# Kernel optimization log

Hardware: AMD Instinct MI355X
Metric: run time of the kernel (lower is better)

The kernel has to match this reference:

```python
import math
import jax, jax.numpy as jnp
import numpy as np

B, S, H, NH = 4, 2048, 1024, 16
HD = H // NH  # 64


def _rope_cos_sin(seq_len, dim, base=10000.0):
    # freqs[j] = base^(-2j/dim), angles = outer(t, freqs)
    inv = 1.0 / (base ** (jnp.arange(0, dim, 2, dtype=jnp.float32) / dim))
    t = jnp.arange(seq_len, dtype=jnp.float32)
    ang = jnp.outer(t, inv)  # (S, dim//2)
    return jnp.cos(ang), jnp.sin(ang)


def _apply_rope(x, cos, sin):
    # x: (B, S, NH, HD); pairs are (x[2i], x[2i+1]) per torch view_as_complex on reshape(..., -1, 2)
    xr = x.reshape(*x.shape[:-1], HD // 2, 2)
    x0, x1 = xr[..., 0], xr[..., 1]
    c = cos[None, :, None, :]  # (1, S, 1, HD//2)
    s = sin[None, :, None, :]
    o0 = x0 * c - x1 * s
    o1 = x0 * s + x1 * c
    return jnp.stack([o0, o1], axis=-1).reshape(x.shape)


def setup_inputs() -> dict:
    key = jax.random.key(0)
    ks = jax.random.split(key, 5)
    scale = 1.0 / math.sqrt(H)
    return {
        "x": jax.random.normal(ks[0], (B, S, H), dtype=jnp.float32),
        "wq": jax.random.normal(ks[1], (H, H), dtype=jnp.float32) * scale,
        "wk": jax.random.normal(ks[2], (H, H), dtype=jnp.float32) * scale,
        "wv": jax.random.normal(ks[3], (H, H), dtype=jnp.float32) * scale,
        "wo": jax.random.normal(ks[4], (H, H), dtype=jnp.float32) * scale,
        "attention_mask": jnp.ones((B, S), dtype=jnp.int32),
    }


def reference(x, wq, wk, wv, wo, attention_mask):
    # Linear(bias=False): y = x @ W.T with W shape (out, in)
    q = jnp.einsum('bsh,oh->bso', x, wq).reshape(B, S, NH, HD)
    k = jnp.einsum('bsh,oh->bso', x, wk).reshape(B, S, NH, HD)
    v = jnp.einsum('bsh,oh->bso', x, wv).reshape(B, S, NH, HD)
    cos, sin = _rope_cos_sin(S, HD)
    q = _apply_rope(q, cos, sin)
    k = _apply_rope(k, cos, sin)
    # scores: (B, NH, S, S)
    scores = jnp.einsum('bqhd,bkhd->bhqk', q, k) / math.sqrt(HD)
    mask = attention_mask[:, None, None, :]  # (B,1,1,S)
    scores = jnp.where(mask == 0, -jnp.inf, scores)
    attn = jax.nn.softmax(scores, axis=-1)
    # attn_dropout: eval mode / p=0 -> identity
    out = jnp.einsum('bhqk,bkhd->bqhd', attn, v).reshape(B, S, H)
    return jnp.einsum('bsh,oh->bso', out, wo)
```

## Files before the change

kernel.cpp:

```cpp
#include <hip/hip_runtime.h>
#include <hip/hip_bf16.h>

#define B_   4
#define S_   2048
#define H_   1024
#define NH_  16
#define HD_  64
#define M_   8192
#define K_   1024

using bf16x8 = __bf16 __attribute__((ext_vector_type(8)));
using f32x4  = float __attribute__((ext_vector_type(4)));
using f32x16 = float __attribute__((ext_vector_type(16)));

__device__ inline f32x4 mfma16(bf16x8 a, bf16x8 b, f32x4 c) {
    return __builtin_amdgcn_mfma_f32_16x16x32_bf16(a, b, c, 0, 0, 0);
}
__device__ inline f32x16 mfma32(bf16x8 a, bf16x8 b, f32x16 c) {
    return __builtin_amdgcn_mfma_f32_32x32x16_bf16(a, b, c, 0, 0, 0);
}

__device__ inline unsigned short f2bf(float f) {
    __hip_bfloat16 h = __float2bfloat16(f);
    return *reinterpret_cast<unsigned short*>(&h);
}

__device__ inline unsigned cvt_pk_bf16(float lo, float hi) {
    unsigned r;
    asm("v_cvt_pk_bf16_f32 %0, %1, %2" : "=v"(r) : "v"(lo), "v"(hi));
    return r;
}

__device__ inline void perm32swap(unsigned &a, unsigned &b) {
    asm("v_permlane32_swap_b32 %0, %1" : "+v"(a), "+v"(b));
}

__device__ inline void gload_lds16(const unsigned short* g, unsigned short* l) {
    __builtin_amdgcn_global_load_lds(
        (const __attribute__((address_space(1))) void*)g,
        (__attribute__((address_space(3))) void*)l, 16, 0, 0);
}

#define EXP2F(x) __builtin_amdgcn_exp2f(x)


__global__ __launch_bounds__(256) void prep_convert(
    const float* __restrict__ x,  const float* __restrict__ wq,
    const float* __restrict__ wk, const float* __restrict__ wv,
    const float* __restrict__ wo, unsigned short* __restrict__ ws,
    const int* __restrict__ mask, float2* __restrict__ ropeb,
    float* __restrict__ biasb, int* __restrict__ kflagb)
{
    size_t u = (size_t)blockIdx.x * 256 + threadIdx.x;
    if (u < 3145728) {
        const float* src; unsigned short* dst; size_t off;
        if (u < 2097152)      { src = x;  dst = ws;            off = u * 4; }
        else if (u < 2359296) { src = wq; dst = ws + 8388608;  off = (u - 2097152) * 4; }
        else if (u < 2621440) { src = wk; dst = ws + 9437184;  off = (u - 2359296) * 4; }
        else if (u < 2883584) { src = wv; dst = ws + 10485760; off = (u - 2621440) * 4; }
        else                  { src = wo; dst = ws + 11534336; off = (u - 2883584) * 4; }
        float4 v = *reinterpret_cast<const float4*>(src + off);
        ushort4 o;
        o.x = f2bf(v.x); o.y = f2bf(v.y); o.z = f2bf(v.z); o.w = f2bf(v.w);
        *reinterpret_cast<ushort4*>(dst + off) = o;
    } else {
        int idx = (int)(u - 3145728);
        int pos = idx >> 5, i = idx & 31;
        float inv = expf(-(float)(2 * i) * (9.210340371976184f / 64.0f));
        float ang = (float)pos * inv;
        float2 cs; cs.x = cosf(ang); cs.y = sinf(ang);
        ropeb[idx] = cs;
        if (idx < B_ * S_)
            biasb[idx] = mask[idx] ? 0.0f : -__builtin_inff();
        if (idx < B_ * 32) {
            int b = idx >> 5, kt = idx & 31;
            int all = 1;
            for (int j = 0; j < 64; j++)
                all &= (mask[b * S_ + kt * 64 + j] != 0) ? 1 : 0;
            kflagb[idx] = all;
        }
    }
}

template<int MODE>
__global__ __launch_bounds__(256, 2) void gemm_main(
    const unsigned short* __restrict__ A,
    const unsigned short* __restrict__ W,
    unsigned short* __restrict__ qbuf, unsigned short* __restrict__ kbuf,
    unsigned short* __restrict__ vtb, float* __restrict__ fout,
    const float* __restrict__ ropeb)
{
    __shared__ alignas(16) unsigned short Al[2][128 * 64];
    __shared__ alignas(16) unsigned short Bl[2][128 * 64];

    const int t = threadIdx.x;
    const int l = t & 63;
    const int w = t >> 6;
    const int lane_r = l & 15, lane_g = l >> 4;
    const int bn = blockIdx.x, bm = blockIdx.y;
    const size_t rowbase = (size_t)bm * 128;
    const int colbase = bn * 128;
    const int wm = (w >> 1) * 64, wn = (w & 1) * 64;
    const int which = (MODE == 0) ? (colbase >> 10) : 3;
    const float scale = (which == 0) ? 0.18033688089184827f : 1.0f;

    const int glrow  = l >> 3;
    const int glslot = (l & 7) ^ glrow;
    const unsigned short* ga = A + (rowbase + w * 8 + glrow) * K_ + glslot * 8;
    const unsigned short* gb = W + (size_t)(colbase + w * 8 + glrow) * K_ + glslot * 8;

#define GLA(bi, kt, i) gload_lds16(ga + (size_t)(i) * 32 * K_ + (kt) * 64, \
                                   &Al[bi][((i) * 32 + w * 8) * 64]);
#define GLB(bi, kt, i) gload_lds16(gb + (size_t)(i) * 32 * K_ + (kt) * 64, \
                                   &Bl[bi][((i) * 32 + w * 8) * 64]);
#define RDA(mt, kk) { int rowa = wm + (mt) * 16 + lane_r;                      \
    af[mt][kk] = *reinterpret_cast<const bf16x8*>((const char*)Al[cur] +       \
        ((rowa * 128 + (kk) * 64 + lane_g * 16) ^ ((rowa & 7) << 4))); }
#define RDB(nt, kk) { int rowb = wn + (nt) * 16 + lane_r;                      \
    bfr[nt][kk] = *reinterpret_cast<const bf16x8*>((const char*)Bl[cur] +      \
        ((rowb * 128 + (kk) * 64 + lane_g * 16) ^ ((rowb & 7) << 4))); }
#define MM(mb, nb)                                                             \
    if (MODE == 0 && which <= 1) {                                             \
        _Pragma("unroll")                                                      \
        for (int a = (nb); a < (nb) + 2; a++)                                  \
            _Pragma("unroll")                                                  \
            for (int b2 = (mb); b2 < (mb) + 2; b2++) {                         \
                acc[a][b2] = mfma16(bfr[a][0], af[b2][0], acc[a][b2]);         \
                acc[a][b2] = mfma16(bfr[a][1], af[b2][1], acc[a][b2]);         \
            }                                                                  \
    } else {                                                                   \
        _Pragma("unroll")                                                      \
        for (int mt = (mb); mt < (mb) + 2; mt++)                               \
            _Pragma("unroll")                                                  \
            for (int nt = (nb); nt < (nb) + 2; nt++) {                         \
                acc[mt][nt] = mfma16(af[mt][0], bfr[nt][0], acc[mt][nt]);      \
                acc[mt][nt] = mfma16(af[mt][1], bfr[nt][1], acc[mt][nt]);      \
            }                                                                  \
    }
#define BARS __builtin_amdgcn_s_barrier();                                     \
             asm volatile("s_waitcnt lgkmcnt(0)" ::: "memory");                \
             __builtin_amdgcn_s_setprio(1);
#define BARE __builtin_amdgcn_s_setprio(0); __builtin_amdgcn_s_barrier();

    f32x4 zero4 = {0.f, 0.f, 0.f, 0.f};
    f32x4 acc[4][4];
#pragma unroll
    for (int a = 0; a < 4; a++)
#pragma unroll
        for (int b2 = 0; b2 < 4; b2++) acc[a][b2] = zero4;

    GLA(0, 0, 0) GLA(0, 0, 1) GLA(0, 0, 2) GLA(0, 0, 3)
    GLB(0, 0, 0) GLB(0, 0, 1) GLB(0, 0, 2) GLB(0, 0, 3)
    __syncthreads();

    for (int kt = 0; kt < 16; kt++) {
        const int cur = kt & 1, nxt = cur ^ 1;
        const bool pf = (kt < 15);
        bf16x8 af[4][2], bfr[4][2];
        RDA(0, 0) RDA(0, 1) RDA(1, 0) RDA(1, 1)
        RDB(0, 0) RDB(0, 1) RDB(1, 0) RDB(1, 1)
        if (pf) { GLA(nxt, kt + 1, 0) GLA(nxt, kt + 1, 1) GLA(nxt, kt + 1, 2) }
        BARS MM(0, 0) BARE
        RDB(2, 0) RDB(2, 1) RDB(3, 0) RDB(3, 1)
        if (pf) { GLA(nxt, kt + 1, 3) GLB(nxt, kt + 1, 0) GLB(nxt, kt + 1, 1) }
        BARS MM(0, 2) BARE
        RDA(2, 0) RDA(2, 1) RDA(3, 0) RDA(3, 1)
        if (pf) { GLB(nxt, kt + 1, 2) GLB(nxt, kt + 1, 3) }
        BARS MM(2, 2) BARE
        __builtin_amdgcn_s_setprio(1);
        MM(2, 0)
        __builtin_amdgcn_s_setprio(0);
        asm volatile("s_waitcnt vmcnt(0)" ::: "memory");
        __builtin_amdgcn_s_barrier();
    }
#undef GLA
#undef GLB
#undef RDA
#undef RDB
#undef MM
#undef BARS
#undef BARE

    if (MODE == 1) {
        float* out = fout;
#pragma unroll
        for (int mt = 0; mt < 4; mt++)
#pragma unroll
            for (int nt = 0; nt < 4; nt++)
#pragma unroll
                for (int i = 0; i < 4; i++) {
                    size_t r = rowbase + wm + mt * 16 + lane_g * 4 + i;
                    int n = colbase + wn + nt * 16 + lane_r;
                    out[r * 1024 + n] = acc[mt][nt][i];
                }
    } else if (which <= 1) {
        unsigned short* out = which ? kbuf : qbuf;
#pragma unroll
        for (int a = 0; a < 4; a++) {
            int nbase = (colbase & 1023) + wn + a * 16 + 4 * lane_g;
            int h = nbase >> 6, d0 = nbase & 63;
#pragma unroll
            for (int b2 = 0; b2 < 4; b2++) {
                size_t r = rowbase + wm + b2 * 16 + lane_r;
                int bb  = (int)(r >> 11);
                int pos = (int)(r & 2047);
                float4 cs = *reinterpret_cast<const float4*>(
                    ropeb + pos * 64 + d0);
                float a0 = acc[a][b2][0], a1 = acc[a][b2][1];
                float a2 = acc[a][b2][2], a3 = acc[a][b2][3];
                float o0 = (a0 * cs.x - a1 * cs.y) * scale;
                float o1 = (a0 * cs.y + a1 * cs.x) * scale;
                float o2 = (a2 * cs.z - a3 * cs.w) * scale;
                float o3 = (a2 * cs.w + a3 * cs.z) * scale;
                uint2 o;
                o.x = cvt_pk_bf16(o0, o1);
                o.y = cvt_pk_bf16(o2, o3);
                *reinterpret_cast<uint2*>(
                    out + (((size_t)(bb * NH_ + h)) * S_ + pos) * 64 + d0) = o;
            }
        }
    } else {
#pragma unroll
        for (int a = 0; a < 4; a++)
#pragma unroll
            for (int b2 = 0; b2 < 4; b2++) {
                size_t rr = rowbase + wm + a * 16 + lane_g * 4;
                int n = (colbase & 1023) + wn + b2 * 16 + lane_r;
                int bb  = (int)(rr >> 11);
                int pos = (int)(rr & 2047);
                int h = n >> 6, d = n & 63;
                ushort4 o;
                o.x = f2bf(acc[a][b2][0]); o.y = f2bf(acc[a][b2][1]);
                o.z = f2bf(acc[a][b2][2]); o.w = f2bf(acc[a][b2][3]);
                *reinterpret_cast<ushort4*>(
                    vtb + (((size_t)(bb * NH_ + h)) * 64 + d) * S_ + pos) = o;
            }
    }
}

__global__ __launch_bounds__(256, 2) void attn_fwd(
    const unsigned short* __restrict__ qb, const unsigned short* __restrict__ kb,
    const unsigned short* __restrict__ vt, const float* __restrict__ biasb,
    const int* __restrict__ kflagb, unsigned short* __restrict__ ao)
{
    __shared__ alignas(16) unsigned short Kl[2][64 * 64];
    __shared__ alignas(16) unsigned short Vl[2][64 * 64];

    const int bid = blockIdx.x;
    const int xcd = bid & 7, idx = bid >> 3;
    const int bh = xcd * 8 + (idx >> 3);
    const int qt = idx & 7;
    const int b = bh >> 4, h = bh & 15;

    const int t = threadIdx.x, l = t & 63, w = t >> 6;
    const int lr = l & 31;
    const int hi = l >> 5;
    const int row8 = lr & 7;

    const unsigned short* qp = qb + (size_t)bh * S_ * 64;
    const unsigned short* kp = kb + (size_t)bh * S_ * 64;
    const unsigned short* vp = vt + (size_t)bh * 64 * S_;
    const float* bp = biasb + (size_t)b * S_;
    const int* kfl = kflagb + b * 32;

    bf16x8 qf[2][4];
#pragma unroll
    for (int qbk = 0; qbk < 2; qbk++) {
        int qrow = qt * 256 + w * 64 + qbk * 32 + lr;
#pragma unroll
        for (int ks = 0; ks < 4; ks++)
            qf[qbk][ks] = *reinterpret_cast<const bf16x8*>(
                qp + (size_t)qrow * 64 + ks * 16 + hi * 8);
    }

    f32x16 zero16;
#pragma unroll
    for (int r = 0; r < 16; r++) zero16[r] = 0.f;

    f32x16 oacc[2][2];
#pragma unroll
    for (int qbk = 0; qbk < 2; qbk++)
#pragma unroll
        for (int r = 0; r < 16; r++) { oacc[qbk][0][r] = 0.f; oacc[qbk][1][r] = 0.f; }
    float lsum[2] = {0.f, 0.f};

    const int grr = l >> 3;
    const int gss = ((l & 7) ^ grr) * 8;

#define STAGE(bi, kt)                                                          \
    {                                                                          \
        _Pragma("unroll")                                                      \
        for (int c = 0; c < 2; c++) {                                          \
            int rbase = w * 16 + c * 8;                                        \
            gload_lds16(kp + (size_t)((kt) * 64 + rbase + grr) * 64 + gss,     \
                        &Kl[bi][rbase * 64]);                                  \
            gload_lds16(vp + (size_t)(rbase + grr) * S_ + (kt) * 64 + gss,     \
                        &Vl[bi][rbase * 64]);                                  \
        }                                                                      \
    }

#define QKBLOCK(C0, C1)                                                        \
    {                                                                          \
        __builtin_amdgcn_s_setprio(1);                                         \
        _Pragma("unroll")                                                      \
        for (int T = 0; T < 2; T++) {                                          \
            int rowb = (32 * T + lr) * 128;                                    \
            bf16x8 kf0 = *reinterpret_cast<const bf16x8*>(                     \
                (const char*)Kl[cur] + rowb + ((hi ^ row8) << 4));             \
            sacc[0][T] = mfma32(kf0, qf[0][0], T ? (C1) : (C0));               \
            sacc[1][T] = mfma32(kf0, qf[1][0], T ? (C1) : (C0));               \
            _Pragma("unroll")                                                  \
            for (int ks = 1; ks < 4; ks++) {                                   \
                bf16x8 kfk = *reinterpret_cast<const bf16x8*>(                 \
                    (const char*)Kl[cur] + rowb + (((2 * ks + hi) ^ row8) << 4)); \
                sacc[0][T] = mfma32(kfk, qf[0][ks], sacc[0][T]);               \
                sacc[1][T] = mfma32(kfk, qf[1][ks], sacc[1][T]);               \
            }                                                                  \
        }                                                                      \
        __builtin_amdgcn_s_setprio(0);                                         \
    }

    STAGE(0, 0)

    for (int kt = 0; kt < 32; kt++) {
        const int cur = kt & 1;
        __syncthreads();
        if (kt < 31) STAGE(cur ^ 1, kt + 1)

        f32x16 sacc[2][2];
        if (kfl[kt]) {
            QKBLOCK(zero16, zero16)
        } else {
            f32x16 binit[2];
#pragma unroll
            for (int T = 0; T < 2; T++)
#pragma unroll
                for (int g = 0; g < 4; g++) {
                    float4 bv = *reinterpret_cast<const float4*>(
                        bp + kt * 64 + T * 32 + g * 8 + hi * 4);
                    binit[T][g * 4 + 0] = bv.x; binit[T][g * 4 + 1] = bv.y;
                    binit[T][g * 4 + 2] = bv.z; binit[T][g * 4 + 3] = bv.w;
                }
            QKBLOCK(binit[0], binit[1])
        }

        bf16x8 pa[2][4];
#pragma unroll
        for (int qbk = 0; qbk < 2; qbk++) {
            unsigned u[2][8];
            float r0 = 0.f, r1 = 0.f, r2 = 0.f, r3 = 0.f;
#pragma unroll
            for (int T = 0; T < 2; T++) {
                float p[16];
#pragma unroll
                for (int r = 0; r < 16; r++) p[r] = EXP2F(sacc[qbk][T][r]);
#pragma unroll
                for (int r = 0; r < 16; r += 4) {
                    r0 += p[r]; r1 += p[r + 1]; r2 += p[r + 2]; r3 += p[r + 3];
                }
#pragma unroll
                for (int bq = 0; bq < 4; bq++) {
                    u[T][bq * 2 + 0] = cvt_pk_bf16(p[bq * 4 + 0], p[bq * 4 + 1]);
                    u[T][bq * 2 + 1] = cvt_pk_bf16(p[bq * 4 + 2], p[bq * 4 + 3]);
                }
            }
            lsum[qbk] += (r0 + r1) + (r2 + r3);
#pragma unroll
            for (int ks = 0; ks < 4; ks++) {
                int T = ks >> 1, e = ks & 1;
                unsigned a0 = u[T][4 * e + 0], b0 = u[T][4 * e + 2];
                unsigned a1 = u[T][4 * e + 1], b1 = u[T][4 * e + 3];
                perm32swap(a0, b0);
                perm32swap(a1, b1);
                unsigned q4[4] = {a0, a1, b0, b1};
                pa[qbk][ks] = *reinterpret_cast<const bf16x8*>(q4);
            }
        }

        __builtin_amdgcn_s_setprio(1);
#pragma unroll
        for (int dt = 0; dt < 2; dt++) {
            int rowb = (32 * dt + lr) * 128;
#pragma unroll
            for (int ks = 0; ks < 4; ks++) {
                bf16x8 vf = *reinterpret_cast<const bf16x8*>(
                    (const char*)Vl[cur] + rowb + (((2 * ks + hi) ^ row8) << 4));
                oacc[0][dt] = mfma32(vf, pa[0][ks], oacc[0][dt]);
                oacc[1][dt] = mfma32(vf, pa[1][ks], oacc[1][dt]);
            }
        }
        __builtin_amdgcn_s_setprio(0);
    }
#undef STAGE
#undef QKBLOCK

#pragma unroll
    for (int qbk = 0; qbk < 2; qbk++) {
        float ls = lsum[qbk];
        ls += __shfl_xor(ls, 32);
        float rl = 1.0f / ls;
        size_t obase = ((size_t)(b * S_) + qt * 256 + w * 64 + qbk * 32 + lr) * 1024 + h * 64;
#pragma unroll
        for (int dt = 0; dt < 2; dt++)
#pragma unroll
            for (int g = 0; g < 4; g++) {
                uint2 o;
                o.x = cvt_pk_bf16(oacc[qbk][dt][g * 4 + 0] * rl, oacc[qbk][dt][g * 4 + 1] * rl);
                o.y = cvt_pk_bf16(oacc[qbk][dt][g * 4 + 2] * rl, oacc[qbk][dt][g * 4 + 3] * rl);
                *reinterpret_cast<uint2*>(ao + obase + 32 * dt + 8 * g + 4 * hi) = o;
            }
    }
}

extern "C" void kernel_launch(void* const* d_in, const int* in_sizes, int n_in,
                              void* d_out, int out_size, void* d_ws, size_t ws_size,
                              hipStream_t stream)
{
    const float* x  = (const float*)d_in[0];
    const float* wq = (const float*)d_in[1];
    const float* wk = (const float*)d_in[2];
    const float* wv = (const float*)d_in[3];
    const float* wo = (const float*)d_in[4];
    const int* mask = (const int*)d_in[5];

    unsigned short* ws   = (unsigned short*)d_ws;
    unsigned short* xb   = ws;
    unsigned short* wqkv = ws + 8388608;
    unsigned short* wob  = ws + 11534336;
    unsigned short* qbuf = ws + 12582912;
    unsigned short* kbuf = ws + 20971520;
    unsigned short* vtb  = ws + 29360128;
    float* ropeb = (float*)(ws + 37748736);
    float* biasb = (float*)(ws + 38010880);
    int* kflagb  = (int*)(biasb + 8192);
    unsigned short* aob = xb;

    prep_convert<<<12544, 256, 0, stream>>>(
        x, wq, wk, wv, wo, ws, mask, (float2*)ropeb, biasb, kflagb);

    gemm_main<0><<<dim3(24, 64), 256, 0, stream>>>(
        xb, wqkv, qbuf, kbuf, vtb, nullptr, ropeb);

    attn_fwd<<<512, 256, 0, stream>>>(qbuf, kbuf, vtb, biasb, kflagb, aob);

    gemm_main<1><<<dim3(8, 64), 256, 0, stream>>>(
        aob, wob, nullptr, nullptr, nullptr, (float*)d_out, nullptr);
}
```

Measured before the change: 198.2 us.

## Split attention work across 8 waves with 32 query rows each

The attention kernel now launches 512 threads per block, so each of 8 waves handles 32 query rows instead of 64. Per-wave register state (Q fragments, score and output accumulators) is halved, and each wave stages a single 8-row chunk of K and V. The mask bias is now added after the QK MFMAs instead of being used as the accumulator initial value. The aim is more waves in flight to hide latency, at the cost of each K/V fragment read from LDS feeding only one MFMA instead of two, which doubles LDS read traffic per unit of compute.

```diff
diff --git a/kernel.cpp b/kernel.cpp
--- a/kernel.cpp
+++ b/kernel.cpp
@@ -238,7 +238,7 @@
     }
 }
 
-__global__ __launch_bounds__(256, 2) void attn_fwd(
+__global__ __launch_bounds__(512, 2) void attn_fwd(
     const unsigned short* __restrict__ qb, const unsigned short* __restrict__ kb,
     const unsigned short* __restrict__ vt, const float* __restrict__ biasb,
     const int* __restrict__ kflagb, unsigned short* __restrict__ ao)
@@ -263,61 +263,30 @@
     const float* bp = biasb + (size_t)b * S_;
     const int* kfl = kflagb + b * 32;
 
-    bf16x8 qf[2][4];
-#pragma unroll
-    for (int qbk = 0; qbk < 2; qbk++) {
-        int qrow = qt * 256 + w * 64 + qbk * 32 + lr;
+    bf16x8 qf[4];
+    {
+        int qrow = qt * 256 + w * 32 + lr;
 #pragma unroll
         for (int ks = 0; ks < 4; ks++)
-            qf[qbk][ks] = *reinterpret_cast<const bf16x8*>(
+            qf[ks] = *reinterpret_cast<const bf16x8*>(
                 qp + (size_t)qrow * 64 + ks * 16 + hi * 8);
     }
 
-    f32x16 zero16;
-#pragma unroll
-    for (int r = 0; r < 16; r++) zero16[r] = 0.f;
-
-    f32x16 oacc[2][2];
-#pragma unroll
-    for (int qbk = 0; qbk < 2; qbk++)
-#pragma unroll
-        for (int r = 0; r < 16; r++) { oacc[qbk][0][r] = 0.f; oacc[qbk][1][r] = 0.f; }
-    float lsum[2] = {0.f, 0.f};
+    f32x16 oacc[2];
+#pragma unroll
+    for (int r = 0; r < 16; r++) { oacc[0][r] = 0.f; oacc[1][r] = 0.f; }
+    float lsum = 0.f;
 
     const int grr = l >> 3;
     const int gss = ((l & 7) ^ grr) * 8;
 
 #define STAGE(bi, kt)                                                          \
     {                                                                          \
-        _Pragma("unroll")                                                      \
-        for (int c = 0; c < 2; c++) {                                          \
-            int rbase = w * 16 + c * 8;                                        \
-            gload_lds16(kp + (size_t)((kt) * 64 + rbase + grr) * 64 + gss,     \
-                        &Kl[bi][rbase * 64]);                                  \
-            gload_lds16(vp + (size_t)(rbase + grr) * S_ + (kt) * 64 + gss,     \
-                        &Vl[bi][rbase * 64]);                                  \
-        }                                                                      \
-    }
-
-#define QKBLOCK(C0, C1)                                                        \
-    {                                                                          \
-        __builtin_amdgcn_s_setprio(1);                                         \
-        _Pragma("unroll")                                                      \
-        for (int T = 0; T < 2; T++) {                                          \
-            int rowb = (32 * T + lr) * 128;                                    \
-            bf16x8 kf0 = *reinterpret_cast<const bf16x8*>(                     \
-                (const char*)Kl[cur] + rowb + ((hi ^ row8) << 4));             \
-            sacc[0][T] = mfma32(kf0, qf[0][0], T ? (C1) : (C0));               \
-            sacc[1][T] = mfma32(kf0, qf[1][0], T ? (C1) : (C0));               \
-            _Pragma("unroll")                                                  \
-            for (int ks = 1; ks < 4; ks++) {                                   \
-                bf16x8 kfk = *reinterpret_cast<const bf16x8*>(                 \
-                    (const char*)Kl[cur] + rowb + (((2 * ks + hi) ^ row8) << 4)); \
-                sacc[0][T] = mfma32(kfk, qf[0][ks], sacc[0][T]);               \
-                sacc[1][T] = mfma32(kfk, qf[1][ks], sacc[1][T]);               \
-            }                                                                  \
-        }                                                                      \
-        __builtin_amdgcn_s_setprio(0);                                         \
+        int rbase = w * 8;                                                     \
+        gload_lds16(kp + (size_t)((kt) * 64 + rbase + grr) * 64 + gss,         \
+                    &Kl[bi][rbase * 64]);                                      \
+        gload_lds16(vp + (size_t)(rbase + grr) * S_ + (kt) * 64 + gss,         \
+                    &Vl[bi][rbase * 64]);                                      \
     }
 
     STAGE(0, 0)
@@ -327,54 +296,68 @@
         __syncthreads();
         if (kt < 31) STAGE(cur ^ 1, kt + 1)
 
-        f32x16 sacc[2][2];
-        if (kfl[kt]) {
-            QKBLOCK(zero16, zero16)
-        } else {
-            f32x16 binit[2];
+        f32x16 sacc[2];
+        {
+            f32x16 zz;
+#pragma unroll
+            for (int r = 0; r < 16; r++) zz[r] = 0.f;
+            __builtin_amdgcn_s_setprio(1);
+#pragma unroll
+            for (int T = 0; T < 2; T++) {
+                int rowb = (32 * T + lr) * 128;
+                bf16x8 kf0 = *reinterpret_cast<const bf16x8*>(
+                    (const char*)Kl[cur] + rowb + ((hi ^ row8) << 4));
+                sacc[T] = mfma32(kf0, qf[0], zz);
+#pragma unroll
+                for (int ks = 1; ks < 4; ks++) {
+                    bf16x8 kfk = *reinterpret_cast<const bf16x8*>(
+                        (const char*)Kl[cur] + rowb + (((2 * ks + hi) ^ row8) << 4));
+                    sacc[T] = mfma32(kfk, qf[ks], sacc[T]);
+                }
+            }
+            __builtin_amdgcn_s_setprio(0);
+        }
+        if (!kfl[kt]) {
 #pragma unroll
             for (int T = 0; T < 2; T++)
 #pragma unroll
                 for (int g = 0; g < 4; g++) {
                     float4 bv = *reinterpret_cast<const float4*>(
                         bp + kt * 64 + T * 32 + g * 8 + hi * 4);
-                    binit[T][g * 4 + 0] = bv.x; binit[T][g * 4 + 1] = bv.y;
-                    binit[T][g * 4 + 2] = bv.z; binit[T][g * 4 + 3] = bv.w;
+                    sacc[T][g * 4 + 0] += bv.x; sacc[T][g * 4 + 1] += bv.y;
+                    sacc[T][g * 4 + 2] += bv.z; sacc[T][g * 4 + 3] += bv.w;
                 }
-            QKBLOCK(binit[0], binit[1])
-        }
-
-        bf16x8 pa[2][4];
-#pragma unroll
-        for (int qbk = 0; qbk < 2; qbk++) {
-            unsigned u[2][8];
-            float r0 = 0.f, r1 = 0.f, r2 = 0.f, r3 = 0.f;
-#pragma unroll
-            for (int T = 0; T < 2; T++) {
-                float p[16];
-#pragma unroll
-                for (int r = 0; r < 16; r++) p[r] = EXP2F(sacc[qbk][T][r]);
-#pragma unroll
-                for (int r = 0; r < 16; r += 4) {
-                    r0 += p[r]; r1 += p[r + 1]; r2 += p[r + 2]; r3 += p[r + 3];
-                }
-#pragma unroll
-                for (int bq = 0; bq < 4; bq++) {
-                    u[T][bq * 2 + 0] = cvt_pk_bf16(p[bq * 4 + 0], p[bq * 4 + 1]);
-                    u[T][bq * 2 + 1] = cvt_pk_bf16(p[bq * 4 + 2], p[bq * 4 + 3]);
-                }
-            }
-            lsum[qbk] += (r0 + r1) + (r2 + r3);
-#pragma unroll
-            for (int ks = 0; ks < 4; ks++) {
-                int T = ks >> 1, e = ks & 1;
-                unsigned a0 = u[T][4 * e + 0], b0 = u[T][4 * e + 2];
-                unsigned a1 = u[T][4 * e + 1], b1 = u[T][4 * e + 3];
-                perm32swap(a0, b0);
-                perm32swap(a1, b1);
-                unsigned q4[4] = {a0, a1, b0, b1};
-                pa[qbk][ks] = *reinterpret_cast<const bf16x8*>(q4);
-            }
+        }
+
+        unsigned u[2][8];
+        float r0 = 0.f, r1 = 0.f, r2 = 0.f, r3 = 0.f;
+#pragma unroll
+        for (int T = 0; T < 2; T++) {
+            float p[16];
+#pragma unroll
+            for (int r = 0; r < 16; r++) p[r] = EXP2F(sacc[T][r]);
+#pragma unroll
+            for (int r = 0; r < 16; r += 4) {
+                r0 += p[r]; r1 += p[r + 1]; r2 += p[r + 2]; r3 += p[r + 3];
+            }
+#pragma unroll
+            for (int bq = 0; bq < 4; bq++) {
+                u[T][bq * 2 + 0] = cvt_pk_bf16(p[bq * 4 + 0], p[bq * 4 + 1]);
+                u[T][bq * 2 + 1] = cvt_pk_bf16(p[bq * 4 + 2], p[bq * 4 + 3]);
+            }
+        }
+        lsum += (r0 + r1) + (r2 + r3);
+
+        bf16x8 pa[4];
+#pragma unroll
+        for (int ks = 0; ks < 4; ks++) {
+            int T = ks >> 1, e = ks & 1;
+            unsigned a0 = u[T][4 * e + 0], b0 = u[T][4 * e + 2];
+            unsigned a1 = u[T][4 * e + 1], b1 = u[T][4 * e + 3];
+            perm32swap(a0, b0);
+            perm32swap(a1, b1);
+            unsigned q4[4] = {a0, a1, b0, b1};
+            pa[ks] = *reinterpret_cast<const bf16x8*>(q4);
         }
 
         __builtin_amdgcn_s_setprio(1);
@@ -385,31 +368,25 @@
             for (int ks = 0; ks < 4; ks++) {
                 bf16x8 vf = *reinterpret_cast<const bf16x8*>(
                     (const char*)Vl[cur] + rowb + (((2 * ks + hi) ^ row8) << 4));
-                oacc[0][dt] = mfma32(vf, pa[0][ks], oacc[0][dt]);
-                oacc[1][dt] = mfma32(vf, pa[1][ks], oacc[1][dt]);
+                oacc[dt] = mfma32(vf, pa[ks], oacc[dt]);
             }
         }
         __builtin_amdgcn_s_setprio(0);
     }
 #undef STAGE
-#undef QKBLOCK
-
-#pragma unroll
-    for (int qbk = 0; qbk < 2; qbk++) {
-        float ls = lsum[qbk];
-        ls += __shfl_xor(ls, 32);
-        float rl = 1.0f / ls;
-        size_t obase = ((size_t)(b * S_) + qt * 256 + w * 64 + qbk * 32 + lr) * 1024 + h * 64;
-#pragma unroll
-        for (int dt = 0; dt < 2; dt++)
-#pragma unroll
-            for (int g = 0; g < 4; g++) {
-                uint2 o;
-                o.x = cvt_pk_bf16(oacc[qbk][dt][g * 4 + 0] * rl, oacc[qbk][dt][g * 4 + 1] * rl);
-                o.y = cvt_pk_bf16(oacc[qbk][dt][g * 4 + 2] * rl, oacc[qbk][dt][g * 4 + 3] * rl);
-                *reinterpret_cast<uint2*>(ao + obase + 32 * dt + 8 * g + 4 * hi) = o;
-            }
-    }
+
+    lsum += __shfl_xor(lsum, 32);
+    float rl = 1.0f / lsum;
+    size_t obase = ((size_t)(b * S_) + qt * 256 + w * 32 + lr) * 1024 + h * 64;
+#pragma unroll
+    for (int dt = 0; dt < 2; dt++)
+#pragma unroll
+        for (int g = 0; g < 4; g++) {
+            uint2 o;
+            o.x = cvt_pk_bf16(oacc[dt][g * 4 + 0] * rl, oacc[dt][g * 4 + 1] * rl);
+            o.y = cvt_pk_bf16(oacc[dt][g * 4 + 2] * rl, oacc[dt][g * 4 + 3] * rl);
+            *reinterpret_cast<uint2*>(ao + obase + 32 * dt + 8 * g + 4 * hi) = o;
+        }
 }
 
 extern "C" void kernel_launch(void* const* d_in, const int* in_sizes, int n_in,
@@ -441,7 +418,7 @@
     gemm_main<0><<<dim3(24, 64), 256, 0, stream>>>(
         xb, wqkv, qbuf, kbuf, vtb, nullptr, ropeb);
 
-    attn_fwd<<<512, 256, 0, stream>>>(qbuf, kbuf, vtb, biasb, kflagb, aob);
+    attn_fwd<<<512, 512, 0, stream>>>(qbuf, kbuf, vtb, biasb, kflagb, aob);
 
     gemm_main<1><<<dim3(8, 64), 256, 0, stream>>>(
         aob, wob, nullptr, nullptr, nullptr, (float*)d_out, nullptr);
```

Result: no change. 194.8 us (-1.7%).
